# Optimization experiments

Measured on AMD Instinct MI355X. Metric: run time of the kernel, lower is better.

The kernel has to match this reference:

```python
import jax, jax.numpy as jnp
import numpy as np

B, N, D = 16, 2048, 64
SCALE = float(np.power(D, 0.5))  # matches np.power(input_dim, 0.5)


def setup_inputs() -> dict:
    key = jax.random.key(0)
    kq, kk, kv = jax.random.split(key, 3)
    Query = jax.random.normal(kq, (B, N, D), dtype=jnp.float32)
    Key = jax.random.normal(kk, (B, N, D), dtype=jnp.float32)
    Value = jax.random.normal(kv, (B, N, D), dtype=jnp.float32)
    # causal 0/1 mask, broadcast to [B, N, N]; guarantees every row has a valid entry
    attn_mask = jnp.broadcast_to(jnp.tril(jnp.ones((N, N), dtype=jnp.float32)), (B, N, N))
    return {"Query": Query, "Key": Key, "Value": Value, "attn_mask": attn_mask}


def reference(Query, Key, Value, attn_mask):
    # scores: [B, N, N]
    att = jnp.einsum("bnd,bmd->bnm", Query, Key) / SCALE
    # multiplicative mask, then masked_fill of exact zeros with -inf (as in torch source)
    att = att * attn_mask
    att = jnp.where(att == 0, -jnp.inf, att)
    att = jax.nn.softmax(att, axis=2)
    outputs = jnp.einsum("bnm,bmd->bnd", att, Value)  # [B, N, D]
    return outputs, att
```

## Files before the change

### kernel.cpp

```cpp
#include <hip/hip_runtime.h>
#include <hip/hip_bf16.h>

#define B_ 16
#define N_ 2048
#define D_ 64

typedef __bf16 bf16x8 __attribute__((ext_vector_type(8)));
typedef __bf16 bf16x4 __attribute__((ext_vector_type(4)));
typedef __bf16 bf16x2 __attribute__((ext_vector_type(2)));
typedef float  f32x4  __attribute__((ext_vector_type(4)));
typedef float  f32x16 __attribute__((ext_vector_type(16)));

static __device__ __forceinline__ bf16x8 ld_frag(const __bf16* p) {
  bf16x4 lo = *(const bf16x4*)p;
  bf16x4 hi = *(const bf16x4*)(p + 4);
  return __builtin_shufflevector(lo, hi, 0, 1, 2, 3, 4, 5, 6, 7);
}

static __device__ __forceinline__ void stage_K(__bf16* dst, int n, int c4,
                                               const f32x4* f) {
  bf16x8 w0, w1;
#pragma unroll
  for (int i = 0; i < 4; ++i) {
    w0[i] = (__bf16)f[0][i]; w0[i + 4] = (__bf16)f[1][i];
    w1[i] = (__bf16)f[2][i]; w1[i + 4] = (__bf16)f[3][i];
  }
  *(bf16x8*)&dst[(2 * c4 + 0) * 512 + n * 8] = w0;
  *(bf16x8*)&dst[(2 * c4 + 1) * 512 + n * 8] = w1;
}

static __device__ __forceinline__ void stage_V(__bf16* dst, int g, int n0,
                                               const f32x4* v) {
#pragma unroll
  for (int p = 0; p < 2; ++p) {
    const int k = 2 * g + 32 * p;
#pragma unroll
    for (int i = 0; i < 4; ++i) {
      bf16x2 pr;
      pr[0] = (__bf16)v[2 * p][i];
      pr[1] = (__bf16)v[2 * p + 1][i];
      *(bf16x2*)&dst[(n0 + i) * 68 + k] = pr;
    }
  }
}

__global__ __launch_bounds__(256, 2)
void General_Attention_62251255988379_kernel(const float* __restrict__ Q,
                                             const float* __restrict__ K,
                                             const float* __restrict__ V,
                                             float* __restrict__ out) {
  __shared__ __bf16 QsL[4096];
  __shared__ __bf16 KsL[2][4096];
  __shared__ __bf16 VtL[2][4352];
  __shared__ __bf16 PtW[4 * 32 * 36];
  __shared__ float  lsum[64];

  const int tid  = threadIdx.x;
  const int blk  = blockIdx.x;
  const int bb   = blk & 15;
  const int u    = blk >> 4;
  const int rb   = (u < 16) ? (31 - u) : (u - 16);
  const int row0 = rb * 64;
  const int lane = tid & 63;
  const int wave = tid >> 6;
  const int wr   = wave & 1;
  const int wc   = wave >> 1;
  const int ln   = lane & 31;
  const int half = lane >> 5;

  const float* Qb = Q + (size_t)bb * N_ * D_;
  const float* Kb = K + (size_t)bb * N_ * D_;
  const float* Vb = V + (size_t)bb * N_ * D_;
  float* Ob = out + (size_t)bb * N_ * D_;
  float* Ab = out + (size_t)B_ * N_ * D_ + (size_t)bb * N_ * N_;

  if (tid < 64) lsum[tid] = 0.0f;

  {
    const int m  = tid >> 2;
    const int c4 = tid & 3;
    const f32x4* src = (const f32x4*)(Qb + (size_t)(row0 + m) * D_ + c4 * 16);
    f32x4 f0 = src[0], f1 = src[1], f2 = src[2], f3 = src[3];
    bf16x8 w0, w1;
#pragma unroll
    for (int i = 0; i < 4; ++i) {
      w0[i]     = (__bf16)(f0[i] * 0.125f);
      w0[i + 4] = (__bf16)(f1[i] * 0.125f);
      w1[i]     = (__bf16)(f2[i] * 0.125f);
      w1[i + 4] = (__bf16)(f3[i] * 0.125f);
    }
    *(bf16x8*)&QsL[(2 * c4 + 0) * 512 + m * 8] = w0;
    *(bf16x8*)&QsL[(2 * c4 + 1) * 512 + m * 8] = w1;
  }
  __syncthreads();

  bf16x8 qf[4];
#pragma unroll
  for (int kk = 0; kk < 4; ++kk)
    qf[kk] = *(const bf16x8*)&QsL[(2 * kk + half) * 512 + (32 * wr + ln) * 8];

  const int n_st = tid >> 2;
  const int c4   = tid & 3;
  const float* Kst = Kb + (size_t)n_st * D_ + c4 * 16;

  f32x4 kp[4];
  {
    const f32x4* kq = (const f32x4*)Kst;
    kp[0] = kq[0]; kp[1] = kq[1]; kp[2] = kq[2]; kp[3] = kq[3];
  }
  stage_K(KsL[0], n_st, c4, kp);

  float sums[16];
#pragma unroll
  for (int r = 0; r < 16; ++r) sums[r] = 0.0f;
  __syncthreads();

#pragma unroll 1
  for (int ct = 0; ct <= rb; ++ct) {
    const int cur = ct & 1;
    if (ct < rb) {
      const f32x4* kq = (const f32x4*)(Kst + (size_t)(ct + 1) * 64 * D_);
      kp[0] = kq[0]; kp[1] = kq[1]; kp[2] = kq[2]; kp[3] = kq[3];
    }
    f32x16 s;
#pragma unroll
    for (int i = 0; i < 16; ++i) s[i] = 0.0f;
#pragma unroll
    for (int kk = 0; kk < 4; ++kk) {
      bf16x8 kf = *(const bf16x8*)&KsL[cur][(2 * kk + half) * 512 + (32 * wc + ln) * 8];
      s = __builtin_amdgcn_mfma_f32_32x32x16_bf16(qf[kk], kf, s, 0, 0, 0);
    }
    const bool diag = (ct == rb);
#pragma unroll
    for (int r = 0; r < 16; ++r) {
      float e = __expf(s[r]);
      if (diag) {
        const int ro = (r & 3) + 8 * (r >> 2) + 4 * half;
        e = ((32 * wc + ln) <= (32 * wr + ro)) ? e : 0.0f;
      }
      sums[r] += e;
    }
    if (ct < rb) stage_K(KsL[cur ^ 1], n_st, c4, kp);
    __syncthreads();
  }

#pragma unroll
  for (int r = 0; r < 16; ++r) {
    float v = sums[r];
    v += __shfl_xor(v, 1);
    v += __shfl_xor(v, 2);
    v += __shfl_xor(v, 4);
    v += __shfl_xor(v, 8);
    v += __shfl_xor(v, 16);
    sums[r] = v;
  }
  if (ln == 0) {
#pragma unroll
    for (int r = 0; r < 16; ++r) {
      const int ro = (r & 3) + 8 * (r >> 2) + 4 * half;
      atomicAdd(&lsum[32 * wr + ro], sums[r]);
    }
  }
  __syncthreads();

  float linv[16];
#pragma unroll
  for (int r = 0; r < 16; ++r) {
    const int ro = (r & 3) + 8 * (r >> 2) + 4 * half;
    linv[r] = 1.0f / lsum[32 * wr + ro];
  }

  const int gV  = tid >> 4;
  const int n0v = (tid & 15) * 4;
  const float* Vst = Vb + (size_t)(2 * gV) * D_ + n0v;

  f32x4 vp[4];
  {
    const f32x4* kq = (const f32x4*)Kst;
    kp[0] = kq[0]; kp[1] = kq[1]; kp[2] = kq[2]; kp[3] = kq[3];
    vp[0] = *(const f32x4*)(Vst);
    vp[1] = *(const f32x4*)(Vst + D_);
    vp[2] = *(const f32x4*)(Vst + 32 * D_);
    vp[3] = *(const f32x4*)(Vst + 33 * D_);
  }
  stage_K(KsL[0], n_st, c4, kp);
  stage_V(VtL[0], gV, n0v, vp);

  f32x16 o0, o1;
#pragma unroll
  for (int i = 0; i < 16; ++i) { o0[i] = 0.0f; o1[i] = 0.0f; }
  __bf16* Pt = &PtW[wave * 32 * 36];
  __syncthreads();

#pragma unroll 1
  for (int ct = 0; ct <= rb; ++ct) {
    const int cur = ct & 1;
    const int c0  = ct * 64;
    if (ct < rb) {
      const size_t off = (size_t)(ct + 1) * 64 * D_;
      const f32x4* kq = (const f32x4*)(Kst + off);
      kp[0] = kq[0]; kp[1] = kq[1]; kp[2] = kq[2]; kp[3] = kq[3];
      vp[0] = *(const f32x4*)(Vst + off);
      vp[1] = *(const f32x4*)(Vst + off + D_);
      vp[2] = *(const f32x4*)(Vst + off + 32 * D_);
      vp[3] = *(const f32x4*)(Vst + off + 33 * D_);
    }
    f32x16 s;
#pragma unroll
    for (int i = 0; i < 16; ++i) s[i] = 0.0f;
#pragma unroll
    for (int kk = 0; kk < 4; ++kk) {
      bf16x8 kf = *(const bf16x8*)&KsL[cur][(2 * kk + half) * 512 + (32 * wc + ln) * 8];
      s = __builtin_amdgcn_mfma_f32_32x32x16_bf16(qf[kk], kf, s, 0, 0, 0);
    }
    const bool diag = (ct == rb);
#pragma unroll
    for (int r = 0; r < 16; ++r) {
      const int ro = (r & 3) + 8 * (r >> 2) + 4 * half;
      float e = __expf(s[r]);
      if (diag) e = ((32 * wc + ln) <= (32 * wr + ro)) ? e : 0.0f;
      const float pv = e * linv[r];
      __builtin_nontemporal_store(pv,
          Ab + (size_t)(row0 + 32 * wr + ro) * N_ + c0 + 32 * wc + ln);
      Pt[ro * 36 + ln] = (__bf16)pv;
    }
#pragma unroll
    for (int kk2 = 0; kk2 < 2; ++kk2) {
      bf16x8 af = ld_frag(&Pt[ln * 36 + 16 * kk2 + 8 * half]);
      bf16x8 b0 = ld_frag(&VtL[cur][ln * 68 + 32 * wc + 16 * kk2 + 8 * half]);
      bf16x8 b1 = ld_frag(&VtL[cur][(32 + ln) * 68 + 32 * wc + 16 * kk2 + 8 * half]);
      o0 = __builtin_amdgcn_mfma_f32_32x32x16_bf16(af, b0, o0, 0, 0, 0);
      o1 = __builtin_amdgcn_mfma_f32_32x32x16_bf16(af, b1, o1, 0, 0, 0);
    }
    if (ct < rb) {
      stage_K(KsL[cur ^ 1], n_st, c4, kp);
      stage_V(VtL[cur ^ 1], gV, n0v, vp);
    }
    __syncthreads();
  }

  float* Ored = (float*)&KsL[0][0];
  if (wc == 1) {
#pragma unroll
    for (int r = 0; r < 16; ++r) {
      const int ro = (r & 3) + 8 * (r >> 2) + 4 * half;
      Ored[(32 * wr + ro) * 64 + ln]      = o0[r];
      Ored[(32 * wr + ro) * 64 + 32 + ln] = o1[r];
    }
  }
  __syncthreads();
  if (wc == 0) {
#pragma unroll
    for (int r = 0; r < 16; ++r) {
      const int ro = (r & 3) + 8 * (r >> 2) + 4 * half;
      float* op = Ob + (size_t)(row0 + 32 * wr + ro) * D_;
      __builtin_nontemporal_store(o0[r] + Ored[(32 * wr + ro) * 64 + ln], op + ln);
      __builtin_nontemporal_store(o1[r] + Ored[(32 * wr + ro) * 64 + 32 + ln], op + 32 + ln);
    }
  }

  const int cz0 = 64 * (rb + 1);
  if (cz0 < N_) {
    f32x4 z = {0.0f, 0.0f, 0.0f, 0.0f};
#pragma unroll 1
    for (int rr = (tid >> 6); rr < 64; rr += 4) {
      float* rowp = Ab + (size_t)(row0 + rr) * N_;
      for (int x = cz0 + (tid & 63) * 4; x < N_; x += 256)
        __builtin_nontemporal_store(z, (f32x4*)(rowp + x));
    }
  }
}

extern "C" void kernel_launch(void* const* d_in, const int* in_sizes, int n_in,
                              void* d_out, int out_size, void* d_ws, size_t ws_size,
                              hipStream_t stream) {
  const float* Q = (const float*)d_in[0];
  const float* K = (const float*)d_in[1];
  const float* V = (const float*)d_in[2];
  (void)in_sizes; (void)n_in; (void)out_size; (void)d_ws; (void)ws_size;
  float* out = (float*)d_out;
  General_Attention_62251255988379_kernel<<<dim3(512), dim3(256), 0, stream>>>(Q, K, V, out);
}
```

Before: 456.6 us.

## Split attention into row-sum and main kernels with key-dimension splitting

The single fused kernel becomes two kernels. The first computes partial softmax row sums with the key tiles split four ways across blocks and writes them to workspace. The second splits the key tiles two ways, combines the partial sums into inverses, and accumulates output rows with float atomics into a zeroed output buffer. It also replaces the loop barrier with an explicit lgkmcnt wait plus s_barrier. This raises grid parallelism and balances the causal triangle better, at the cost of two memsets, an extra launch, recomputing QK^T in both passes, and atomic accumulation that makes results order-dependent.

```diff
diff --git a/kernel.cpp b/kernel.cpp
--- a/kernel.cpp
+++ b/kernel.cpp
@@ -4,6 +4,7 @@
 #define B_ 16
 #define N_ 2048
 #define D_ 64
+#define BN_ (B_ * N_)
 
 typedef __bf16 bf16x8 __attribute__((ext_vector_type(8)));
 typedef __bf16 bf16x4 __attribute__((ext_vector_type(4)));
@@ -44,23 +45,27 @@
   }
 }
 
-__global__ __launch_bounds__(256, 2)
-void General_Attention_62251255988379_kernel(const float* __restrict__ Q,
-                                             const float* __restrict__ K,
-                                             const float* __restrict__ V,
-                                             float* __restrict__ out) {
+static __device__ __forceinline__ void barrier_lgkm() {
+  asm volatile("s_waitcnt lgkmcnt(0)" ::: "memory");
+  __builtin_amdgcn_s_barrier();
+  asm volatile("" ::: "memory");
+}
+
+__global__ __launch_bounds__(256, 4)
+void attn_sums_kernel(const float* __restrict__ Q, const float* __restrict__ K,
+                      float* __restrict__ lpart_g) {
   __shared__ __bf16 QsL[4096];
   __shared__ __bf16 KsL[2][4096];
-  __shared__ __bf16 VtL[2][4352];
-  __shared__ __bf16 PtW[4 * 32 * 36];
-  __shared__ float  lsum[64];
-
-  const int tid  = threadIdx.x;
-  const int blk  = blockIdx.x;
-  const int bb   = blk & 15;
-  const int u    = blk >> 4;
-  const int rb   = (u < 16) ? (31 - u) : (u - 16);
-  const int row0 = rb * 64;
+  __shared__ float  lpart[2][64];
+
+  const int tid = threadIdx.x;
+  const int blk = blockIdx.x;
+  const int bb  = blk & 15;
+  const int idx = blk >> 4;
+  const int rt  = 31 - (idx >> 2);
+  const int q   = idx & 3;
+  if (q > rt) return;
+  const int row0 = rt * 64;
   const int lane = tid & 63;
   const int wave = tid >> 6;
   const int wr   = wave & 1;
@@ -70,16 +75,11 @@
 
   const float* Qb = Q + (size_t)bb * N_ * D_;
   const float* Kb = K + (size_t)bb * N_ * D_;
-  const float* Vb = V + (size_t)bb * N_ * D_;
-  float* Ob = out + (size_t)bb * N_ * D_;
-  float* Ab = out + (size_t)B_ * N_ * D_ + (size_t)bb * N_ * N_;
-
-  if (tid < 64) lsum[tid] = 0.0f;
 
   {
-    const int m  = tid >> 2;
-    const int c4 = tid & 3;
-    const f32x4* src = (const f32x4*)(Qb + (size_t)(row0 + m) * D_ + c4 * 16);
+    const int m   = tid >> 2;
+    const int c4q = tid & 3;
+    const f32x4* src = (const f32x4*)(Qb + (size_t)(row0 + m) * D_ + c4q * 16);
     f32x4 f0 = src[0], f1 = src[1], f2 = src[2], f3 = src[3];
     bf16x8 w0, w1;
 #pragma unroll
@@ -89,8 +89,8 @@
       w1[i]     = (__bf16)(f2[i] * 0.125f);
       w1[i + 4] = (__bf16)(f3[i] * 0.125f);
     }
-    *(bf16x8*)&QsL[(2 * c4 + 0) * 512 + m * 8] = w0;
-    *(bf16x8*)&QsL[(2 * c4 + 1) * 512 + m * 8] = w1;
+    *(bf16x8*)&QsL[(2 * c4q + 0) * 512 + m * 8] = w0;
+    *(bf16x8*)&QsL[(2 * c4q + 1) * 512 + m * 8] = w1;
   }
   __syncthreads();
 
@@ -103,9 +103,10 @@
   const int c4   = tid & 3;
   const float* Kst = Kb + (size_t)n_st * D_ + c4 * 16;
 
+  const int nt = (rt - q) / 4 + 1;
   f32x4 kp[4];
   {
-    const f32x4* kq = (const f32x4*)Kst;
+    const f32x4* kq = (const f32x4*)(Kst + (size_t)q * 64 * D_);
     kp[0] = kq[0]; kp[1] = kq[1]; kp[2] = kq[2]; kp[3] = kq[3];
   }
   stage_K(KsL[0], n_st, c4, kp);
@@ -116,21 +117,22 @@
   __syncthreads();
 
 #pragma unroll 1
-  for (int ct = 0; ct <= rb; ++ct) {
-    const int cur = ct & 1;
-    if (ct < rb) {
-      const f32x4* kq = (const f32x4*)(Kst + (size_t)(ct + 1) * 64 * D_);
+  for (int i = 0; i < nt; ++i) {
+    const int ct  = q + 4 * i;
+    const int cur = i & 1;
+    if (i + 1 < nt) {
+      const f32x4* kq = (const f32x4*)(Kst + (size_t)(ct + 4) * 64 * D_);
       kp[0] = kq[0]; kp[1] = kq[1]; kp[2] = kq[2]; kp[3] = kq[3];
     }
     f32x16 s;
 #pragma unroll
-    for (int i = 0; i < 16; ++i) s[i] = 0.0f;
+    for (int j = 0; j < 16; ++j) s[j] = 0.0f;
 #pragma unroll
     for (int kk = 0; kk < 4; ++kk) {
       bf16x8 kf = *(const bf16x8*)&KsL[cur][(2 * kk + half) * 512 + (32 * wc + ln) * 8];
       s = __builtin_amdgcn_mfma_f32_32x32x16_bf16(qf[kk], kf, s, 0, 0, 0);
     }
-    const bool diag = (ct == rb);
+    const bool diag = (ct == rt);
 #pragma unroll
     for (int r = 0; r < 16; ++r) {
       float e = __expf(s[r]);
@@ -140,8 +142,8 @@
       }
       sums[r] += e;
     }
-    if (ct < rb) stage_K(KsL[cur ^ 1], n_st, c4, kp);
-    __syncthreads();
+    if (i + 1 < nt) stage_K(KsL[cur ^ 1], n_st, c4, kp);
+    barrier_lgkm();
   }
 
 #pragma unroll
@@ -158,114 +160,187 @@
 #pragma unroll
     for (int r = 0; r < 16; ++r) {
       const int ro = (r & 3) + 8 * (r >> 2) + 4 * half;
-      atomicAdd(&lsum[32 * wr + ro], sums[r]);
+      lpart[wc][32 * wr + ro] = sums[r];
     }
   }
   __syncthreads();
-
-  float linv[16];
-#pragma unroll
-  for (int r = 0; r < 16; ++r) {
-    const int ro = (r & 3) + 8 * (r >> 2) + 4 * half;
-    linv[r] = 1.0f / lsum[32 * wr + ro];
-  }
-
-  const int gV  = tid >> 4;
-  const int n0v = (tid & 15) * 4;
-  const float* Vst = Vb + (size_t)(2 * gV) * D_ + n0v;
-
-  f32x4 vp[4];
-  {
-    const f32x4* kq = (const f32x4*)Kst;
-    kp[0] = kq[0]; kp[1] = kq[1]; kp[2] = kq[2]; kp[3] = kq[3];
-    vp[0] = *(const f32x4*)(Vst);
-    vp[1] = *(const f32x4*)(Vst + D_);
-    vp[2] = *(const f32x4*)(Vst + 32 * D_);
-    vp[3] = *(const f32x4*)(Vst + 33 * D_);
-  }
-  stage_K(KsL[0], n_st, c4, kp);
-  stage_V(VtL[0], gV, n0v, vp);
-
-  f32x16 o0, o1;
-#pragma unroll
-  for (int i = 0; i < 16; ++i) { o0[i] = 0.0f; o1[i] = 0.0f; }
-  __bf16* Pt = &PtW[wave * 32 * 36];
-  __syncthreads();
-
-#pragma unroll 1
-  for (int ct = 0; ct <= rb; ++ct) {
-    const int cur = ct & 1;
-    const int c0  = ct * 64;
-    if (ct < rb) {
-      const size_t off = (size_t)(ct + 1) * 64 * D_;
-      const f32x4* kq = (const f32x4*)(Kst + off);
-      kp[0] = kq[0]; kp[1] = kq[1]; kp[2] = kq[2]; kp[3] = kq[3];
-      vp[0] = *(const f32x4*)(Vst + off);
-      vp[1] = *(const f32x4*)(Vst + off + D_);
-      vp[2] = *(const f32x4*)(Vst + off + 32 * D_);
-      vp[3] = *(const f32x4*)(Vst + off + 33 * D_);
-    }
-    f32x16 s;
-#pragma unroll
-    for (int i = 0; i < 16; ++i) s[i] = 0.0f;
-#pragma unroll
-    for (int kk = 0; kk < 4; ++kk) {
-      bf16x8 kf = *(const bf16x8*)&KsL[cur][(2 * kk + half) * 512 + (32 * wc + ln) * 8];
-      s = __builtin_amdgcn_mfma_f32_32x32x16_bf16(qf[kk], kf, s, 0, 0, 0);
-    }
-    const bool diag = (ct == rb);
+  if (tid < 64)
+    lpart_g[(size_t)q * BN_ + (size_t)bb * N_ + row0 + tid] =
+        lpart[0][tid] + lpart[1][tid];
+}
+
+__global__ __launch_bounds__(256, 3)
+void attn_main_kernel(const float* __restrict__ Q, const float* __restrict__ K,
+                      const float* __restrict__ V, float* __restrict__ out,
+                      const float* __restrict__ lpart_g) {
+  __shared__ __bf16 QsL[4096];
+  __shared__ __bf16 KsL[2][4096];
+  __shared__ __bf16 VtL[2][4352];
+  __shared__ __bf16 PtW[4 * 32 * 36];
+  __shared__ float  linvL[64];
+
+  const int tid = threadIdx.x;
+  const int blk = blockIdx.x;
+  const int bb  = blk & 15;
+  const int idx = blk >> 4;
+  const int rt  = 31 - (idx >> 1);
+  const int par = idx & 1;
+  const int row0 = rt * 64;
+  const int lane = tid & 63;
+  const int wave = tid >> 6;
+  const int wr   = wave & 1;
+  const int wc   = wave >> 1;
+  const int ln   = lane & 31;
+  const int half = lane >> 5;
+
+  const float* Qb = Q + (size_t)bb * N_ * D_;
+  const float* Kb = K + (size_t)bb * N_ * D_;
+  const float* Vb = V + (size_t)bb * N_ * D_;
+  float* Ob = out + (size_t)bb * N_ * D_;
+  float* Ab = out + (size_t)B_ * N_ * D_ + (size_t)bb * N_ * N_;
+
+  const int nt = (rt >= par) ? ((rt - par) >> 1) + 1 : 0;
+
+  if (nt > 0) {
+    if (tid < 64) {
+      const size_t base = (size_t)bb * N_ + row0 + tid;
+      float t = ((lpart_g[base] + lpart_g[(size_t)BN_ + base]) +
+                 lpart_g[2 * (size_t)BN_ + base]) +
+                lpart_g[3 * (size_t)BN_ + base];
+      linvL[tid] = 1.0f / t;
+    }
+    {
+      const int m   = tid >> 2;
+      const int c4q = tid & 3;
+      const f32x4* src = (const f32x4*)(Qb + (size_t)(row0 + m) * D_ + c4q * 16);
+      f32x4 f0 = src[0], f1 = src[1], f2 = src[2], f3 = src[3];
+      bf16x8 w0, w1;
+#pragma unroll
+      for (int i = 0; i < 4; ++i) {
+        w0[i]     = (__bf16)(f0[i] * 0.125f);
+        w0[i + 4] = (__bf16)(f1[i] * 0.125f);
+        w1[i]     = (__bf16)(f2[i] * 0.125f);
+        w1[i + 4] = (__bf16)(f3[i] * 0.125f);
+      }
+      *(bf16x8*)&QsL[(2 * c4q + 0) * 512 + m * 8] = w0;
+      *(bf16x8*)&QsL[(2 * c4q + 1) * 512 + m * 8] = w1;
+    }
+    __syncthreads();
+
+    bf16x8 qf[4];
+#pragma unroll
+    for (int kk = 0; kk < 4; ++kk)
+      qf[kk] = *(const bf16x8*)&QsL[(2 * kk + half) * 512 + (32 * wr + ln) * 8];
+
+    float linv[16];
 #pragma unroll
     for (int r = 0; r < 16; ++r) {
       const int ro = (r & 3) + 8 * (r >> 2) + 4 * half;
-      float e = __expf(s[r]);
-      if (diag) e = ((32 * wc + ln) <= (32 * wr + ro)) ? e : 0.0f;
-      const float pv = e * linv[r];
-      __builtin_nontemporal_store(pv,
-          Ab + (size_t)(row0 + 32 * wr + ro) * N_ + c0 + 32 * wc + ln);
-      Pt[ro * 36 + ln] = (__bf16)pv;
-    }
-#pragma unroll
-    for (int kk2 = 0; kk2 < 2; ++kk2) {
-      bf16x8 af = ld_frag(&Pt[ln * 36 + 16 * kk2 + 8 * half]);
-      bf16x8 b0 = ld_frag(&VtL[cur][ln * 68 + 32 * wc + 16 * kk2 + 8 * half]);
-      bf16x8 b1 = ld_frag(&VtL[cur][(32 + ln) * 68 + 32 * wc + 16 * kk2 + 8 * half]);
-      o0 = __builtin_amdgcn_mfma_f32_32x32x16_bf16(af, b0, o0, 0, 0, 0);
-      o1 = __builtin_amdgcn_mfma_f32_32x32x16_bf16(af, b1, o1, 0, 0, 0);
-    }
-    if (ct < rb) {
-      stage_K(KsL[cur ^ 1], n_st, c4, kp);
-      stage_V(VtL[cur ^ 1], gV, n0v, vp);
-    }
+      linv[r] = linvL[32 * wr + ro];
+    }
+
+    const int n_st = tid >> 2;
+    const int c4   = tid & 3;
+    const float* Kst = Kb + (size_t)n_st * D_ + c4 * 16;
+    const int gV  = tid >> 4;
+    const int n0v = (tid & 15) * 4;
+    const float* Vst = Vb + (size_t)(2 * gV) * D_ + n0v;
+
+    f32x4 kp[4], vp[4];
+    {
+      const size_t off0 = (size_t)par * 64 * D_;
+      const f32x4* kq = (const f32x4*)(Kst + off0);
+      kp[0] = kq[0]; kp[1] = kq[1]; kp[2] = kq[2]; kp[3] = kq[3];
+      vp[0] = *(const f32x4*)(Vst + off0);
+      vp[1] = *(const f32x4*)(Vst + off0 + D_);
+      vp[2] = *(const f32x4*)(Vst + off0 + 32 * D_);
+      vp[3] = *(const f32x4*)(Vst + off0 + 33 * D_);
+    }
+    stage_K(KsL[0], n_st, c4, kp);
+    stage_V(VtL[0], gV, n0v, vp);
+
+    f32x16 o0, o1;
+#pragma unroll
+    for (int i = 0; i < 16; ++i) { o0[i] = 0.0f; o1[i] = 0.0f; }
+    __bf16* Pt = &PtW[wave * 32 * 36];
     __syncthreads();
-  }
-
-  float* Ored = (float*)&KsL[0][0];
-  if (wc == 1) {
-#pragma unroll
-    for (int r = 0; r < 16; ++r) {
-      const int ro = (r & 3) + 8 * (r >> 2) + 4 * half;
-      Ored[(32 * wr + ro) * 64 + ln]      = o0[r];
-      Ored[(32 * wr + ro) * 64 + 32 + ln] = o1[r];
-    }
-  }
-  __syncthreads();
-  if (wc == 0) {
-#pragma unroll
-    for (int r = 0; r < 16; ++r) {
-      const int ro = (r & 3) + 8 * (r >> 2) + 4 * half;
-      float* op = Ob + (size_t)(row0 + 32 * wr + ro) * D_;
-      __builtin_nontemporal_store(o0[r] + Ored[(32 * wr + ro) * 64 + ln], op + ln);
-      __builtin_nontemporal_store(o1[r] + Ored[(32 * wr + ro) * 64 + 32 + ln], op + 32 + ln);
-    }
-  }
-
-  const int cz0 = 64 * (rb + 1);
+
+#pragma unroll 1
+    for (int i = 0; i < nt; ++i) {
+      const int ct  = par + 2 * i;
+      const int cur = i & 1;
+      const int c0  = ct * 64;
+      if (i + 1 < nt) {
+        const size_t off = (size_t)(ct + 2) * 64 * D_;
+        const f32x4* kq = (const f32x4*)(Kst + off);
+        kp[0] = kq[0]; kp[1] = kq[1]; kp[2] = kq[2]; kp[3] = kq[3];
+        vp[0] = *(const f32x4*)(Vst + off);
+        vp[1] = *(const f32x4*)(Vst + off + D_);
+        vp[2] = *(const f32x4*)(Vst + off + 32 * D_);
+        vp[3] = *(const f32x4*)(Vst + off + 33 * D_);
+      }
+      f32x16 s;
+#pragma unroll
+      for (int j = 0; j < 16; ++j) s[j] = 0.0f;
+#pragma unroll
+      for (int kk = 0; kk < 4; ++kk) {
+        bf16x8 kf = *(const bf16x8*)&KsL[cur][(2 * kk + half) * 512 + (32 * wc + ln) * 8];
+        s = __builtin_amdgcn_mfma_f32_32x32x16_bf16(qf[kk], kf, s, 0, 0, 0);
+      }
+      const bool diag = (ct == rt);
+#pragma unroll
+      for (int r = 0; r < 16; ++r) {
+        const int ro = (r & 3) + 8 * (r >> 2) + 4 * half;
+        float e = __expf(s[r]);
+        if (diag) e = ((32 * wc + ln) <= (32 * wr + ro)) ? e : 0.0f;
+        const float pv = e * linv[r];
+        __builtin_nontemporal_store(pv,
+            Ab + (size_t)(row0 + 32 * wr + ro) * N_ + c0 + 32 * wc + ln);
+        Pt[ro * 36 + ln] = (__bf16)pv;
+      }
+#pragma unroll
+      for (int kk2 = 0; kk2 < 2; ++kk2) {
+        bf16x8 af = ld_frag(&Pt[ln * 36 + 16 * kk2 + 8 * half]);
+        bf16x8 b0 = ld_frag(&VtL[cur][ln * 68 + 32 * wc + 16 * kk2 + 8 * half]);
+        bf16x8 b1 = ld_frag(&VtL[cur][(32 + ln) * 68 + 32 * wc + 16 * kk2 + 8 * half]);
+        o0 = __builtin_amdgcn_mfma_f32_32x32x16_bf16(af, b0, o0, 0, 0, 0);
+        o1 = __builtin_amdgcn_mfma_f32_32x32x16_bf16(af, b1, o1, 0, 0, 0);
+      }
+      if (i + 1 < nt) {
+        stage_K(KsL[cur ^ 1], n_st, c4, kp);
+        stage_V(VtL[cur ^ 1], gV, n0v, vp);
+      }
+      barrier_lgkm();
+    }
+
+    float* Ored = (float*)&KsL[0][0];
+    if (wc == 1) {
+#pragma unroll
+      for (int r = 0; r < 16; ++r) {
+        const int ro = (r & 3) + 8 * (r >> 2) + 4 * half;
+        Ored[(32 * wr + ro) * 64 + ln]      = o0[r];
+        Ored[(32 * wr + ro) * 64 + 32 + ln] = o1[r];
+      }
+    }
+    __syncthreads();
+    if (wc == 0) {
+#pragma unroll
+      for (int r = 0; r < 16; ++r) {
+        const int ro = (r & 3) + 8 * (r >> 2) + 4 * half;
+        float* op = Ob + (size_t)(row0 + 32 * wr + ro) * D_;
+        unsafeAtomicAdd(op + ln,      o0[r] + Ored[(32 * wr + ro) * 64 + ln]);
+        unsafeAtomicAdd(op + 32 + ln, o1[r] + Ored[(32 * wr + ro) * 64 + 32 + ln]);
+      }
+    }
+  }
+
+  const int cz0 = 64 * (rt + 1);
   if (cz0 < N_) {
     f32x4 z = {0.0f, 0.0f, 0.0f, 0.0f};
 #pragma unroll 1
     for (int rr = (tid >> 6); rr < 64; rr += 4) {
       float* rowp = Ab + (size_t)(row0 + rr) * N_;
-      for (int x = cz0 + (tid & 63) * 4; x < N_; x += 256)
+      for (int x = cz0 + (tid & 63) * 4 + par * 256; x < N_; x += 512)
         __builtin_nontemporal_store(z, (f32x4*)(rowp + x));
     }
   }
@@ -277,7 +352,13 @@
   const float* Q = (const float*)d_in[0];
   const float* K = (const float*)d_in[1];
   const float* V = (const float*)d_in[2];
-  (void)in_sizes; (void)n_in; (void)out_size; (void)d_ws; (void)ws_size;
+  (void)in_sizes; (void)n_in; (void)out_size; (void)ws_size;
   float* out = (float*)d_out;
-  General_Attention_62251255988379_kernel<<<dim3(512), dim3(256), 0, stream>>>(Q, K, V, out);
-}
+  float* ws  = (float*)d_ws;
+
+  hipMemsetAsync(d_ws, 0, (size_t)4 * BN_ * sizeof(float), stream);
+  hipMemsetAsync(d_out, 0, (size_t)B_ * N_ * D_ * sizeof(float), stream);
+
+  attn_sums_kernel<<<dim3(2048), dim3(256), 0, stream>>>(Q, K, ws);
+  attn_main_kernel<<<dim3(1024), dim3(256), 0, stream>>>(Q, K, V, out, ws);
+}
```

New measurement: 463.9 us. Within noise of the previous version (+1.6%).

## Prefetch K/V two tiles ahead with register double-buffering and LDS-only barriers

Applied to the files above, without the earlier changes.

Restructures both the row-sum pass and the output pass into a manually unrolled two-phase loop. Two register sets (A/B) hold K and V tiles fetched two iterations ahead, and each tile is staged into LDS one iteration before use, so global load latency has a full iteration to resolve. __syncthreads is replaced by a barrier that waits only on lgkmcnt, so outstanding global loads no longer stall at the barrier. This costs extra registers for the second prefetch buffer, which could hurt occupancy at launch bounds of 2 blocks per CU. It also relies on the staging writes being correctly ordered against reads through the lgkm wait.

```diff
diff --git a/kernel.cpp b/kernel.cpp
--- a/kernel.cpp
+++ b/kernel.cpp
@@ -41,6 +41,80 @@
       pr[1] = (__bf16)v[2 * p + 1][i];
       *(bf16x2*)&dst[(n0 + i) * 68 + k] = pr;
     }
+  }
+}
+
+static __device__ __forceinline__ void barrier_lgkm() {
+  asm volatile("s_waitcnt lgkmcnt(0)" ::: "memory");
+  __builtin_amdgcn_s_barrier();
+  asm volatile("" ::: "memory");
+}
+
+static __device__ __forceinline__ void loadK16(const float* p, size_t off, f32x4* kp) {
+  const f32x4* kq = (const f32x4*)(p + off);
+  kp[0] = kq[0]; kp[1] = kq[1]; kp[2] = kq[2]; kp[3] = kq[3];
+}
+static __device__ __forceinline__ void loadV16(const float* p, size_t off, f32x4* vp) {
+  vp[0] = *(const f32x4*)(p + off);
+  vp[1] = *(const f32x4*)(p + off + D_);
+  vp[2] = *(const f32x4*)(p + off + 32 * D_);
+  vp[3] = *(const f32x4*)(p + off + 33 * D_);
+}
+
+static __device__ __forceinline__ void passA_tile(const __bf16* Ks, const bf16x8* qf,
+                                                  int wr, int wc, int ln, int half,
+                                                  bool diag, float* sums) {
+  f32x16 s;
+#pragma unroll
+  for (int j = 0; j < 16; ++j) s[j] = 0.0f;
+#pragma unroll
+  for (int kk = 0; kk < 4; ++kk) {
+    bf16x8 kf = *(const bf16x8*)&Ks[(2 * kk + half) * 512 + (32 * wc + ln) * 8];
+    s = __builtin_amdgcn_mfma_f32_32x32x16_bf16(qf[kk], kf, s, 0, 0, 0);
+  }
+#pragma unroll
+  for (int r = 0; r < 16; ++r) {
+    float e = __expf(s[r]);
+    if (diag) {
+      const int ro = (r & 3) + 8 * (r >> 2) + 4 * half;
+      e = ((32 * wc + ln) <= (32 * wr + ro)) ? e : 0.0f;
+    }
+    sums[r] += e;
+  }
+}
+
+static __device__ __forceinline__ void passB_tile(const __bf16* Ks, const __bf16* Vt,
+                                                  __bf16* Pt, const bf16x8* qf,
+                                                  const float* linv, float* Ab,
+                                                  int row0, int ct, bool diag,
+                                                  int wr, int wc, int ln, int half,
+                                                  f32x16& o0, f32x16& o1) {
+  const int c0 = ct * 64;
+  f32x16 s;
+#pragma unroll
+  for (int j = 0; j < 16; ++j) s[j] = 0.0f;
+#pragma unroll
+  for (int kk = 0; kk < 4; ++kk) {
+    bf16x8 kf = *(const bf16x8*)&Ks[(2 * kk + half) * 512 + (32 * wc + ln) * 8];
+    s = __builtin_amdgcn_mfma_f32_32x32x16_bf16(qf[kk], kf, s, 0, 0, 0);
+  }
+#pragma unroll
+  for (int r = 0; r < 16; ++r) {
+    const int ro = (r & 3) + 8 * (r >> 2) + 4 * half;
+    float e = __expf(s[r]);
+    if (diag) e = ((32 * wc + ln) <= (32 * wr + ro)) ? e : 0.0f;
+    const float pv = e * linv[r];
+    __builtin_nontemporal_store(pv,
+        Ab + (size_t)(row0 + 32 * wr + ro) * N_ + c0 + 32 * wc + ln);
+    Pt[ro * 36 + ln] = (__bf16)pv;
+  }
+#pragma unroll
+  for (int kk2 = 0; kk2 < 2; ++kk2) {
+    bf16x8 af = ld_frag(&Pt[ln * 36 + 16 * kk2 + 8 * half]);
+    bf16x8 b0 = ld_frag(&Vt[ln * 68 + 32 * wc + 16 * kk2 + 8 * half]);
+    bf16x8 b1 = ld_frag(&Vt[(32 + ln) * 68 + 32 * wc + 16 * kk2 + 8 * half]);
+    o0 = __builtin_amdgcn_mfma_f32_32x32x16_bf16(af, b0, o0, 0, 0, 0);
+    o1 = __builtin_amdgcn_mfma_f32_32x32x16_bf16(af, b1, o1, 0, 0, 0);
   }
 }
 
@@ -78,8 +152,8 @@
 
   {
     const int m  = tid >> 2;
-    const int c4 = tid & 3;
-    const f32x4* src = (const f32x4*)(Qb + (size_t)(row0 + m) * D_ + c4 * 16);
+    const int c4q = tid & 3;
+    const f32x4* src = (const f32x4*)(Qb + (size_t)(row0 + m) * D_ + c4q * 16);
     f32x4 f0 = src[0], f1 = src[1], f2 = src[2], f3 = src[3];
     bf16x8 w0, w1;
 #pragma unroll
@@ -89,8 +163,8 @@
       w1[i]     = (__bf16)(f2[i] * 0.125f);
       w1[i + 4] = (__bf16)(f3[i] * 0.125f);
     }
-    *(bf16x8*)&QsL[(2 * c4 + 0) * 512 + m * 8] = w0;
-    *(bf16x8*)&QsL[(2 * c4 + 1) * 512 + m * 8] = w1;
+    *(bf16x8*)&QsL[(2 * c4q + 0) * 512 + m * 8] = w0;
+    *(bf16x8*)&QsL[(2 * c4q + 1) * 512 + m * 8] = w1;
   }
   __syncthreads();
 
@@ -102,13 +176,12 @@
   const int n_st = tid >> 2;
   const int c4   = tid & 3;
   const float* Kst = Kb + (size_t)n_st * D_ + c4 * 16;
-
-  f32x4 kp[4];
-  {
-    const f32x4* kq = (const f32x4*)Kst;
-    kp[0] = kq[0]; kp[1] = kq[1]; kp[2] = kq[2]; kp[3] = kq[3];
-  }
-  stage_K(KsL[0], n_st, c4, kp);
+  const int nt = rb + 1;
+
+  f32x4 kpA[4], kpB[4];
+  loadK16(Kst, 0, kpA);
+  stage_K(KsL[0], n_st, c4, kpA);
+  if (nt > 1) loadK16(Kst, (size_t)64 * D_, kpB);
 
   float sums[16];
 #pragma unroll
@@ -116,32 +189,17 @@
   __syncthreads();
 
 #pragma unroll 1
-  for (int ct = 0; ct <= rb; ++ct) {
-    const int cur = ct & 1;
-    if (ct < rb) {
-      const f32x4* kq = (const f32x4*)(Kst + (size_t)(ct + 1) * 64 * D_);
-      kp[0] = kq[0]; kp[1] = kq[1]; kp[2] = kq[2]; kp[3] = kq[3];
-    }
-    f32x16 s;
-#pragma unroll
-    for (int i = 0; i < 16; ++i) s[i] = 0.0f;
-#pragma unroll
-    for (int kk = 0; kk < 4; ++kk) {
-      bf16x8 kf = *(const bf16x8*)&KsL[cur][(2 * kk + half) * 512 + (32 * wc + ln) * 8];
-      s = __builtin_amdgcn_mfma_f32_32x32x16_bf16(qf[kk], kf, s, 0, 0, 0);
-    }
-    const bool diag = (ct == rb);
-#pragma unroll
-    for (int r = 0; r < 16; ++r) {
-      float e = __expf(s[r]);
-      if (diag) {
-        const int ro = (r & 3) + 8 * (r >> 2) + 4 * half;
-        e = ((32 * wc + ln) <= (32 * wr + ro)) ? e : 0.0f;
-      }
-      sums[r] += e;
-    }
-    if (ct < rb) stage_K(KsL[cur ^ 1], n_st, c4, kp);
-    __syncthreads();
+  for (int i = 0; i < nt; ) {
+    if (i + 1 < nt) stage_K(KsL[1], n_st, c4, kpB);
+    if (i + 2 < nt) loadK16(Kst, (size_t)(i + 2) * 64 * D_, kpA);
+    passA_tile(KsL[0], qf, wr, wc, ln, half, i == rb, sums);
+    barrier_lgkm();
+    if (++i >= nt) break;
+    if (i + 1 < nt) stage_K(KsL[0], n_st, c4, kpA);
+    if (i + 2 < nt) loadK16(Kst, (size_t)(i + 2) * 64 * D_, kpB);
+    passA_tile(KsL[1], qf, wr, wc, ln, half, i == rb, sums);
+    barrier_lgkm();
+    ++i;
   }
 
 #pragma unroll
@@ -174,17 +232,15 @@
   const int n0v = (tid & 15) * 4;
   const float* Vst = Vb + (size_t)(2 * gV) * D_ + n0v;
 
-  f32x4 vp[4];
-  {
-    const f32x4* kq = (const f32x4*)Kst;
-    kp[0] = kq[0]; kp[1] = kq[1]; kp[2] = kq[2]; kp[3] = kq[3];
-    vp[0] = *(const f32x4*)(Vst);
-    vp[1] = *(const f32x4*)(Vst + D_);
-    vp[2] = *(const f32x4*)(Vst + 32 * D_);
-    vp[3] = *(const f32x4*)(Vst + 33 * D_);
-  }
-  stage_K(KsL[0], n_st, c4, kp);
-  stage_V(VtL[0], gV, n0v, vp);
+  f32x4 vpA[4], vpB[4];
+  loadK16(Kst, 0, kpA);
+  loadV16(Vst, 0, vpA);
+  stage_K(KsL[0], n_st, c4, kpA);
+  stage_V(VtL[0], gV, n0v, vpA);
+  if (nt > 1) {
+    loadK16(Kst, (size_t)64 * D_, kpB);
+    loadV16(Vst, (size_t)64 * D_, vpB);
+  }
 
   f32x16 o0, o1;
 #pragma unroll
@@ -193,50 +249,31 @@
   __syncthreads();
 
 #pragma unroll 1
-  for (int ct = 0; ct <= rb; ++ct) {
-    const int cur = ct & 1;
-    const int c0  = ct * 64;
-    if (ct < rb) {
-      const size_t off = (size_t)(ct + 1) * 64 * D_;
-      const f32x4* kq = (const f32x4*)(Kst + off);
-      kp[0] = kq[0]; kp[1] = kq[1]; kp[2] = kq[2]; kp[3] = kq[3];
-      vp[0] = *(const f32x4*)(Vst + off);
-      vp[1] = *(const f32x4*)(Vst + off + D_);
-      vp[2] = *(const f32x4*)(Vst + off + 32 * D_);
-      vp[3] = *(const f32x4*)(Vst + off + 33 * D_);
-    }
-    f32x16 s;
-#pragma unroll
-    for (int i = 0; i < 16; ++i) s[i] = 0.0f;
-#pragma unroll
-    for (int kk = 0; kk < 4; ++kk) {
-      bf16x8 kf = *(const bf16x8*)&KsL[cur][(2 * kk + half) * 512 + (32 * wc + ln) * 8];
-      s = __builtin_amdgcn_mfma_f32_32x32x16_bf16(qf[kk], kf, s, 0, 0, 0);
-    }
-    const bool diag = (ct == rb);
-#pragma unroll
-    for (int r = 0; r < 16; ++r) {
-      const int ro = (r & 3) + 8 * (r >> 2) + 4 * half;
-      float e = __expf(s[r]);
-      if (diag) e = ((32 * wc + ln) <= (32 * wr + ro)) ? e : 0.0f;
-      const float pv = e * linv[r];
-      __builtin_nontemporal_store(pv,
-          Ab + (size_t)(row0 + 32 * wr + ro) * N_ + c0 + 32 * wc + ln);
-      Pt[ro * 36 + ln] = (__bf16)pv;
-    }
-#pragma unroll
-    for (int kk2 = 0; kk2 < 2; ++kk2) {
-      bf16x8 af = ld_frag(&Pt[ln * 36 + 16 * kk2 + 8 * half]);
-      bf16x8 b0 = ld_frag(&VtL[cur][ln * 68 + 32 * wc + 16 * kk2 + 8 * half]);
-      bf16x8 b1 = ld_frag(&VtL[cur][(32 + ln) * 68 + 32 * wc + 16 * kk2 + 8 * half]);
-      o0 = __builtin_amdgcn_mfma_f32_32x32x16_bf16(af, b0, o0, 0, 0, 0);
-      o1 = __builtin_amdgcn_mfma_f32_32x32x16_bf16(af, b1, o1, 0, 0, 0);
-    }
-    if (ct < rb) {
-      stage_K(KsL[cur ^ 1], n_st, c4, kp);
-      stage_V(VtL[cur ^ 1], gV, n0v, vp);
-    }
-    __syncthreads();
+  for (int i = 0; i < nt; ) {
+    if (i + 1 < nt) {
+      stage_K(KsL[1], n_st, c4, kpB);
+      stage_V(VtL[1], gV, n0v, vpB);
+    }
+    if (i + 2 < nt) {
+      loadK16(Kst, (size_t)(i + 2) * 64 * D_, kpA);
+      loadV16(Vst, (size_t)(i + 2) * 64 * D_, vpA);
+    }
+    passB_tile(KsL[0], VtL[0], Pt, qf, linv, Ab, row0, i, i == rb,
+               wr, wc, ln, half, o0, o1);
+    barrier_lgkm();
+    if (++i >= nt) break;
+    if (i + 1 < nt) {
+      stage_K(KsL[0], n_st, c4, kpA);
+      stage_V(VtL[0], gV, n0v, vpA);
+    }
+    if (i + 2 < nt) {
+      loadK16(Kst, (size_t)(i + 2) * 64 * D_, kpB);
+      loadV16(Vst, (size_t)(i + 2) * 64 * D_, vpB);
+    }
+    passB_tile(KsL[1], VtL[1], Pt, qf, linv, Ab, row0, i, i == rb,
+               wr, wc, ln, half, o0, o1);
+    barrier_lgkm();
+    ++i;
   }
 
   float* Ored = (float*)&KsL[0][0];
```

Measured after the change: 455.3 us. No clear change (-0.3%).

## Give each wave private K/V staging to drop block-wide barriers in attention loops

Applied to the files above, without the earlier changes.

Each wave now loads and converts its own 32-key slice of K and V into wave-private LDS buffers, so the per-tile __syncthreads in both the row-sum pass and the output pass can be removed. Loads are prefetched two tiles ahead in registers, and the transposed V layout uses an XOR swizzle to reduce bank conflicts. In exchange, the two waves sharing a column slice each load the same K/V data, so global traffic and register pressure go up, and correctness now depends on ordering within a wave.

```diff
diff --git a/kernel.cpp b/kernel.cpp
--- a/kernel.cpp
+++ b/kernel.cpp
@@ -4,10 +4,11 @@
 #define B_ 16
 #define N_ 2048
 #define D_ 64
+#define KCS 264
+#define VTS 36
 
 typedef __bf16 bf16x8 __attribute__((ext_vector_type(8)));
 typedef __bf16 bf16x4 __attribute__((ext_vector_type(4)));
-typedef __bf16 bf16x2 __attribute__((ext_vector_type(2)));
 typedef float  f32x4  __attribute__((ext_vector_type(4)));
 typedef float  f32x16 __attribute__((ext_vector_type(16)));
 
@@ -17,30 +18,33 @@
   return __builtin_shufflevector(lo, hi, 0, 1, 2, 3, 4, 5, 6, 7);
 }
 
-static __device__ __forceinline__ void stage_K(__bf16* dst, int n, int c4,
-                                               const f32x4* f) {
-  bf16x8 w0, w1;
-#pragma unroll
-  for (int i = 0; i < 4; ++i) {
-    w0[i] = (__bf16)f[0][i]; w0[i + 4] = (__bf16)f[1][i];
-    w1[i] = (__bf16)f[2][i]; w1[i + 4] = (__bf16)f[3][i];
-  }
-  *(bf16x8*)&dst[(2 * c4 + 0) * 512 + n * 8] = w0;
-  *(bf16x8*)&dst[(2 * c4 + 1) * 512 + n * 8] = w1;
-}
-
-static __device__ __forceinline__ void stage_V(__bf16* dst, int g, int n0,
-                                               const f32x4* v) {
-#pragma unroll
-  for (int p = 0; p < 2; ++p) {
-    const int k = 2 * g + 32 * p;
-#pragma unroll
-    for (int i = 0; i < 4; ++i) {
-      bf16x2 pr;
-      pr[0] = (__bf16)v[2 * p][i];
-      pr[1] = (__bf16)v[2 * p + 1][i];
-      *(bf16x2*)&dst[(n0 + i) * 68 + k] = pr;
-    }
+static __device__ __forceinline__ void loadT(const float* base, int lane, f32x4* r) {
+#pragma unroll
+  for (int j = 0; j < 8; ++j)
+    r[j] = *(const f32x4*)(base + j * 256 + lane * 4);
+}
+
+static __device__ __forceinline__ void stageKw(__bf16* Kp, int lane, const f32x4* r) {
+  __bf16* dst = &Kp[((lane & 15) >> 1) * KCS + (lane >> 4) * 8 + (lane & 1) * 4];
+#pragma unroll
+  for (int j = 0; j < 8; ++j) {
+    bf16x4 w;
+#pragma unroll
+    for (int i = 0; i < 4; ++i) w[i] = (__bf16)r[j][i];
+    *(bf16x4*)&dst[j * 32] = w;
+  }
+}
+
+static __device__ __forceinline__ void stageVw(__bf16* Vt, int lane, const f32x4* r) {
+  const int d0 = (lane & 15) * 4;
+  const int r0 = lane >> 4;
+  const int sw = ((lane & 15) >> 2) << 3;
+#pragma unroll
+  for (int j = 0; j < 8; ++j) {
+    const int k = (4 * j + r0) ^ sw;
+#pragma unroll
+    for (int i = 0; i < 4; ++i)
+      Vt[(d0 + i) * VTS + k] = (__bf16)r[j][i];
   }
 }
 
@@ -50,8 +54,8 @@
                                              const float* __restrict__ V,
                                              float* __restrict__ out) {
   __shared__ __bf16 QsL[4096];
-  __shared__ __bf16 KsL[2][4096];
-  __shared__ __bf16 VtL[2][4352];
+  __shared__ __bf16 KpL[4 * 8 * KCS];
+  __shared__ __bf16 VtL[2][4 * 64 * VTS];
   __shared__ __bf16 PtW[4 * 32 * 36];
   __shared__ float  lsum[64];
 
@@ -77,9 +81,9 @@
   if (tid < 64) lsum[tid] = 0.0f;
 
   {
-    const int m  = tid >> 2;
-    const int c4 = tid & 3;
-    const f32x4* src = (const f32x4*)(Qb + (size_t)(row0 + m) * D_ + c4 * 16);
+    const int m   = tid >> 2;
+    const int c4q = tid & 3;
+    const f32x4* src = (const f32x4*)(Qb + (size_t)(row0 + m) * D_ + c4q * 16);
     f32x4 f0 = src[0], f1 = src[1], f2 = src[2], f3 = src[3];
     bf16x8 w0, w1;
 #pragma unroll
@@ -89,8 +93,8 @@
       w1[i]     = (__bf16)(f2[i] * 0.125f);
       w1[i + 4] = (__bf16)(f3[i] * 0.125f);
     }
-    *(bf16x8*)&QsL[(2 * c4 + 0) * 512 + m * 8] = w0;
-    *(bf16x8*)&QsL[(2 * c4 + 1) * 512 + m * 8] = w1;
+    *(bf16x8*)&QsL[(2 * c4q + 0) * 512 + m * 8] = w0;
+    *(bf16x8*)&QsL[(2 * c4q + 1) * 512 + m * 8] = w1;
   }
   __syncthreads();
 
@@ -99,38 +103,35 @@
   for (int kk = 0; kk < 4; ++kk)
     qf[kk] = *(const bf16x8*)&QsL[(2 * kk + half) * 512 + (32 * wr + ln) * 8];
 
-  const int n_st = tid >> 2;
-  const int c4   = tid & 3;
-  const float* Kst = Kb + (size_t)n_st * D_ + c4 * 16;
-
-  f32x4 kp[4];
-  {
-    const f32x4* kq = (const f32x4*)Kst;
-    kp[0] = kq[0]; kp[1] = kq[1]; kp[2] = kq[2]; kp[3] = kq[3];
-  }
-  stage_K(KsL[0], n_st, c4, kp);
+  const int nt = rb + 1;
+  __bf16* Kp = &KpL[wave * 8 * KCS];
+  const float* KtB = Kb + (size_t)(32 * wc) * D_;
+  const float* VtB = Vb + (size_t)(32 * wc) * D_;
+
+  f32x4 kraw[8];
+  loadT(KtB, lane, kraw);
+  stageKw(Kp, lane, kraw);
+  if (nt > 1) loadT(KtB + (size_t)64 * D_, lane, kraw);
 
   float sums[16];
 #pragma unroll
   for (int r = 0; r < 16; ++r) sums[r] = 0.0f;
-  __syncthreads();
 
 #pragma unroll 1
-  for (int ct = 0; ct <= rb; ++ct) {
-    const int cur = ct & 1;
-    if (ct < rb) {
-      const f32x4* kq = (const f32x4*)(Kst + (size_t)(ct + 1) * 64 * D_);
-      kp[0] = kq[0]; kp[1] = kq[1]; kp[2] = kq[2]; kp[3] = kq[3];
-    }
+  for (int i = 0; i < nt; ++i) {
+    bf16x8 kf[4];
+#pragma unroll
+    for (int kk = 0; kk < 4; ++kk)
+      kf[kk] = *(const bf16x8*)&Kp[(2 * kk + half) * KCS + ln * 8];
+    if (i + 1 < nt) stageKw(Kp, lane, kraw);
+    if (i + 2 < nt) loadT(KtB + (size_t)(i + 2) * 64 * D_, lane, kraw);
     f32x16 s;
 #pragma unroll
-    for (int i = 0; i < 16; ++i) s[i] = 0.0f;
-#pragma unroll
-    for (int kk = 0; kk < 4; ++kk) {
-      bf16x8 kf = *(const bf16x8*)&KsL[cur][(2 * kk + half) * 512 + (32 * wc + ln) * 8];
-      s = __builtin_amdgcn_mfma_f32_32x32x16_bf16(qf[kk], kf, s, 0, 0, 0);
-    }
-    const bool diag = (ct == rb);
+    for (int j = 0; j < 16; ++j) s[j] = 0.0f;
+#pragma unroll
+    for (int kk = 0; kk < 4; ++kk)
+      s = __builtin_amdgcn_mfma_f32_32x32x16_bf16(qf[kk], kf[kk], s, 0, 0, 0);
+    const bool diag = (i == rb);
 #pragma unroll
     for (int r = 0; r < 16; ++r) {
       float e = __expf(s[r]);
@@ -140,8 +141,6 @@
       }
       sums[r] += e;
     }
-    if (ct < rb) stage_K(KsL[cur ^ 1], n_st, c4, kp);
-    __syncthreads();
   }
 
 #pragma unroll
@@ -170,50 +169,44 @@
     linv[r] = 1.0f / lsum[32 * wr + ro];
   }
 
-  const int gV  = tid >> 4;
-  const int n0v = (tid & 15) * 4;
-  const float* Vst = Vb + (size_t)(2 * gV) * D_ + n0v;
-
-  f32x4 vp[4];
-  {
-    const f32x4* kq = (const f32x4*)Kst;
-    kp[0] = kq[0]; kp[1] = kq[1]; kp[2] = kq[2]; kp[3] = kq[3];
-    vp[0] = *(const f32x4*)(Vst);
-    vp[1] = *(const f32x4*)(Vst + D_);
-    vp[2] = *(const f32x4*)(Vst + 32 * D_);
-    vp[3] = *(const f32x4*)(Vst + 33 * D_);
-  }
-  stage_K(KsL[0], n_st, c4, kp);
-  stage_V(VtL[0], gV, n0v, vp);
+  f32x4 vraw[8];
+  loadT(KtB, lane, kraw);
+  loadT(VtB, lane, vraw);
+  stageKw(Kp, lane, kraw);
+  stageVw(&VtL[0][wave * 64 * VTS], lane, vraw);
+  if (nt > 1) {
+    loadT(KtB + (size_t)64 * D_, lane, kraw);
+    loadT(VtB + (size_t)64 * D_, lane, vraw);
+  }
 
   f32x16 o0, o1;
 #pragma unroll
   for (int i = 0; i < 16; ++i) { o0[i] = 0.0f; o1[i] = 0.0f; }
   __bf16* Pt = &PtW[wave * 32 * 36];
-  __syncthreads();
+  const int sw0 = ((ln >> 4) & 1) << 3;
 
 #pragma unroll 1
-  for (int ct = 0; ct <= rb; ++ct) {
-    const int cur = ct & 1;
-    const int c0  = ct * 64;
-    if (ct < rb) {
-      const size_t off = (size_t)(ct + 1) * 64 * D_;
-      const f32x4* kq = (const f32x4*)(Kst + off);
-      kp[0] = kq[0]; kp[1] = kq[1]; kp[2] = kq[2]; kp[3] = kq[3];
-      vp[0] = *(const f32x4*)(Vst + off);
-      vp[1] = *(const f32x4*)(Vst + off + D_);
-      vp[2] = *(const f32x4*)(Vst + off + 32 * D_);
-      vp[3] = *(const f32x4*)(Vst + off + 33 * D_);
+  for (int i = 0; i < nt; ++i) {
+    bf16x8 kf[4];
+#pragma unroll
+    for (int kk = 0; kk < 4; ++kk)
+      kf[kk] = *(const bf16x8*)&Kp[(2 * kk + half) * KCS + ln * 8];
+    if (i + 1 < nt) {
+      stageKw(Kp, lane, kraw);
+      stageVw(&VtL[(i + 1) & 1][wave * 64 * VTS], lane, vraw);
+    }
+    if (i + 2 < nt) {
+      loadT(KtB + (size_t)(i + 2) * 64 * D_, lane, kraw);
+      loadT(VtB + (size_t)(i + 2) * 64 * D_, lane, vraw);
     }
     f32x16 s;
 #pragma unroll
-    for (int i = 0; i < 16; ++i) s[i] = 0.0f;
-#pragma unroll
-    for (int kk = 0; kk < 4; ++kk) {
-      bf16x8 kf = *(const bf16x8*)&KsL[cur][(2 * kk + half) * 512 + (32 * wc + ln) * 8];
-      s = __builtin_amdgcn_mfma_f32_32x32x16_bf16(qf[kk], kf, s, 0, 0, 0);
-    }
-    const bool diag = (ct == rb);
+    for (int j = 0; j < 16; ++j) s[j] = 0.0f;
+#pragma unroll
+    for (int kk = 0; kk < 4; ++kk)
+      s = __builtin_amdgcn_mfma_f32_32x32x16_bf16(qf[kk], kf[kk], s, 0, 0, 0);
+    const bool diag = (i == rb);
+    const int  c0   = i * 64;
 #pragma unroll
     for (int r = 0; r < 16; ++r) {
       const int ro = (r & 3) + 8 * (r >> 2) + 4 * half;
@@ -224,22 +217,20 @@
           Ab + (size_t)(row0 + 32 * wr + ro) * N_ + c0 + 32 * wc + ln);
       Pt[ro * 36 + ln] = (__bf16)pv;
     }
+    const __bf16* Vtc = &VtL[i & 1][wave * 64 * VTS];
 #pragma unroll
     for (int kk2 = 0; kk2 < 2; ++kk2) {
-      bf16x8 af = ld_frag(&Pt[ln * 36 + 16 * kk2 + 8 * half]);
-      bf16x8 b0 = ld_frag(&VtL[cur][ln * 68 + 32 * wc + 16 * kk2 + 8 * half]);
-      bf16x8 b1 = ld_frag(&VtL[cur][(32 + ln) * 68 + 32 * wc + 16 * kk2 + 8 * half]);
+      const int koff = 16 * kk2 + 8 * half;
+      bf16x8 af = ld_frag(&Pt[ln * 36 + koff]);
+      bf16x8 b0 = ld_frag(&Vtc[ln * VTS + (koff ^ sw0)]);
+      bf16x8 b1 = ld_frag(&Vtc[(32 + ln) * VTS + (koff ^ sw0 ^ 16)]);
       o0 = __builtin_amdgcn_mfma_f32_32x32x16_bf16(af, b0, o0, 0, 0, 0);
       o1 = __builtin_amdgcn_mfma_f32_32x32x16_bf16(af, b1, o1, 0, 0, 0);
     }
-    if (ct < rb) {
-      stage_K(KsL[cur ^ 1], n_st, c4, kp);
-      stage_V(VtL[cur ^ 1], gV, n0v, vp);
-    }
-    __syncthreads();
-  }
-
-  float* Ored = (float*)&KsL[0][0];
+  }
+
+  __syncthreads();
+  float* Ored = (float*)&KpL[0];
   if (wc == 1) {
 #pragma unroll
     for (int r = 0; r < 16; ++r) {
```

Result: slower. 467.1 us (+2.3%).
